# Kernel optimization log

Measured on AMD Instinct MI355X. Metric: run time of the kernel, lower is better.

Reference implementation:

```python
import jax, jax.numpy as jnp
import numpy as np

SCALE = 1.0  # alpha / rank = 32 / 32


def setup_inputs() -> dict:
    key = jax.random.key(0)
    k_x, k_w, k_b, k_a, k_bb = jax.random.split(key, 5)
    B, S, D = 4, 4096, 3072
    depth, rank = 4, 32
    x = jax.random.normal(k_x, (B, S, D), dtype=jnp.float32)
    W = jax.random.normal(k_w, (D, D), dtype=jnp.float32) * (1.0 / np.sqrt(D))
    b = jax.random.normal(k_b, (D,), dtype=jnp.float32) * 0.02
    lora_A = jax.random.normal(k_a, (depth, rank, D), dtype=jnp.float32) * (1.0 / np.sqrt(D))
    lora_B = jax.random.normal(k_bb, (depth, D, rank), dtype=jnp.float32) * 0.02
    return {"x": x, "W": W, "b": b, "lora_A": lora_A, "lora_B": lora_B}


def reference(x, W, b, lora_A, lora_B):
    # base: y = x @ W.T + b
    base_out = jnp.einsum('bsi,oi->bso', x, W) + b
    # stacked LoRA: sum_d (x @ A_d.T @ B_d.T); dropout=0 -> identity
    # down-project to rank per depth: [B,S,depth,rank]
    z = jnp.einsum('bsi,dri->bsdr', x, lora_A)
    lora_out = jnp.einsum('bsdr,dor->bso', z, lora_B)
    return base_out + lora_out * SCALE
```

## Files before the change

### kernel.cpp

```cpp
#include <hip/hip_runtime.h>
#include <hip/hip_bf16.h>


typedef unsigned short ushort_t;
typedef short bf16x8 __attribute__((ext_vector_type(8)));
typedef float floatx4 __attribute__((ext_vector_type(4)));
typedef unsigned short ushortx4 __attribute__((ext_vector_type(4)));
typedef unsigned short ushortx8 __attribute__((ext_vector_type(8)));

__device__ __forceinline__ ushort_t f2bf(float f) {
    __hip_bfloat16 h = __float2bfloat16(f);
    return *(ushort_t*)&h;
}

__device__ __forceinline__ void async_load16(const void* g, void* l) {
    __builtin_amdgcn_global_load_lds(
        (const __attribute__((address_space(1))) void*)g,
        (__attribute__((address_space(3))) void*)l,
        16, 0, 0);
}

#define MFMA16(a, b, c) __builtin_amdgcn_mfma_f32_16x16x32_bf16(a, b, c, 0, 0, 0)

__global__ __launch_bounds__(256)
void cvt_kernel(const float* __restrict__ in, ushort_t* __restrict__ out, int n8) {
    int i = blockIdx.x * 256 + threadIdx.x;
    if (i < n8) {
        const float4 v0 = ((const float4*)in)[2 * i];
        const float4 v1 = ((const float4*)in)[2 * i + 1];
        ushortx8 o = { f2bf(v0.x), f2bf(v0.y), f2bf(v0.z), f2bf(v0.w),
                       f2bf(v1.x), f2bf(v1.y), f2bf(v1.z), f2bf(v1.w) };
        ((ushortx8*)out)[i] = o;
    }
}

__global__ __launch_bounds__(256)
void transpose_lora_kernel(const float* __restrict__ lb,
                           const float* __restrict__ la,
                           ushort_t* __restrict__ outB,
                           ushort_t* __restrict__ outA) {
    int bid = blockIdx.x;
    if (bid < 1536) {
        int idx = bid * 256 + threadIdx.x;
        int n = idx >> 7;
        int j = idx & 127;
        int d = j >> 5, r = j & 31;
        outB[idx] = f2bf(lb[(size_t)d * (3072 * 32) + (size_t)n * 32 + r]);
    } else {
        int idx = (bid - 1536) * 256 + threadIdx.x;
        int kk = idx >> 7;
        int j  = idx & 127;
        outA[idx] = f2bf(la[(size_t)j * 3072 + kk]);
    }
}

template <int KT, bool OUT_F32, bool ADD_MAT>
__global__ __launch_bounds__(256)
void gemm_bt_kernel(const ushort_t* __restrict__ A, int lda,
                    const ushort_t* __restrict__ B, int ldb,
                    const float* __restrict__ Cadd,
                    const float* __restrict__ bias,
                    void* __restrict__ Cv, int ldc)
{
    __shared__ ushort_t As[128 * 32];
    __shared__ ushort_t Bs[128 * 32];

    const int t    = threadIdx.x;
    const int lane = t & 63;
    const int wave = t >> 6;
    const int wr   = wave >> 1, wc = wave & 1;
    const int quad = lane >> 4, l16 = lane & 15;

    const int mBase = blockIdx.y * 128;
    const int nBase = blockIdx.x * 128;

    floatx4 acc[4][4] = {};

    const int p0 = t,       r0 = p0 >> 2, g0 = ((p0 & 3) ^ ((r0 >> 1) & 3)) << 3;
    const int p1 = t + 256, r1 = p1 >> 2, g1 = ((p1 & 3) ^ ((r1 >> 1) & 3)) << 3;
    const int qs = (quad ^ ((l16 >> 1) & 3)) << 3;

    for (int kt = 0; kt < KT; ++kt) {
        const int ko = kt * 32;

        async_load16(A + (size_t)(mBase + r0) * lda + ko + g0, &As[p0 * 8]);
        async_load16(A + (size_t)(mBase + r1) * lda + ko + g1, &As[p1 * 8]);
        async_load16(B + (size_t)(nBase + r0) * ldb + ko + g0, &Bs[p0 * 8]);
        async_load16(B + (size_t)(nBase + r1) * ldb + ko + g1, &Bs[p1 * 8]);

        __syncthreads();

        bf16x8 af[4], bf[4];
#pragma unroll
        for (int mi = 0; mi < 4; ++mi)
            af[mi] = *(const bf16x8*)&As[(wr * 64 + mi * 16 + l16) * 32 + qs];
#pragma unroll
        for (int ni = 0; ni < 4; ++ni)
            bf[ni] = *(const bf16x8*)&Bs[(wc * 64 + ni * 16 + l16) * 32 + qs];

#pragma unroll
        for (int mi = 0; mi < 4; ++mi)
#pragma unroll
            for (int ni = 0; ni < 4; ++ni)
                acc[mi][ni] = MFMA16(af[mi], bf[ni], acc[mi][ni]);

        __syncthreads();
    }

#pragma unroll
    for (int ni = 0; ni < 4; ++ni) {
        const int col = nBase + wc * 64 + ni * 16 + l16;
        const float bv = bias ? bias[col] : 0.0f;
#pragma unroll
        for (int mi = 0; mi < 4; ++mi) {
            const int row = mBase + wr * 64 + mi * 16 + quad * 4;
#pragma unroll
            for (int r = 0; r < 4; ++r) {
                float v = acc[mi][ni][r] + bv;
                if (ADD_MAT) v += Cadd[(size_t)(row + r) * ldc + col];
                if (OUT_F32) {
                    ((float*)Cv)[(size_t)(row + r) * ldc + col] = v;
                } else {
                    ((ushort_t*)Cv)[(size_t)(row + r) * ldc + col] = f2bf(v);
                }
            }
        }
    }
}

__global__ __launch_bounds__(512)
void gemm256_kernel(const ushort_t* __restrict__ A,
                    const ushort_t* __restrict__ B,
                    const float* __restrict__ bias,
                    float* __restrict__ C)
{
    constexpr int LDA = 3072;
    constexpr int NT  = 48;
    constexpr int NBX = 12;

    __shared__ ushort_t smem_u[81920];
    char* const smem = (char*)smem_u;

    const int t    = threadIdx.x;
    const int lane = t & 63;
    const int wave = t >> 6;
    const int wr   = wave >> 2;
    const int wc   = wave & 3;
    const int quad = lane >> 4;
    const int l16  = lane & 15;

    const int bid = blockIdx.x;
    const int sw  = (bid & 7) * 96 + (bid >> 3);
    const int bx  = sw % NBX;
    const int by  = sw / NBX;
    const int mBase = by * 256;
    const int nBase = bx * 256;

    const int prow = t >> 3;
    const int cg   = (t & 7) ^ (prow & 7);
    const ushort_t* const aSrc = A + (size_t)(mBase + prow) * LDA + cg * 8;
    const ushort_t* const bSrc = B + (size_t)(nBase + prow) * LDA + cg * 8;

#define STAGE_A(off, h, ktv) do {                                           \
        const ushort_t* _s = aSrc + (size_t)(h) * 128 * LDA + (ktv) * 64;   \
        char* _d = smem + (off) + (h) * 16384 + t * 16;                     \
        async_load16(_s, _d);                                               \
        async_load16(_s + 64 * LDA, _d + 8192);                             \
    } while (0)
#define STAGE_B(off, h, ktv) do {                                           \
        const ushort_t* _s = bSrc + (size_t)(h) * 128 * LDA + (ktv) * 64;   \
        char* _d = smem + (off) + (h) * 16384 + t * 16;                     \
        async_load16(_s, _d);                                               \
        async_load16(_s + 64 * LDA, _d + 8192);                             \
    } while (0)

    const int s0  = ((0 + quad) ^ (l16 & 7)) << 4;
    const int s1  = ((4 + quad) ^ (l16 & 7)) << 4;
    const int aRdB = wr * 16384 + l16 * 128;
    const int bRdB = (wc >> 1) * 16384 + ((wc & 1) * 64 + l16) * 128;

    floatx4 acc[8][4] = {};
    bf16x8 af[8][2];
    bf16x8 bfr[4][2];

    STAGE_A(0,      0, 0); STAGE_A(0,      1, 0);
    STAGE_B(65536,  0, 0); STAGE_B(65536,  1, 0);
    STAGE_A(32768,  0, 1); STAGE_A(32768,  1, 1);
    STAGE_B(98304,  0, 1); STAGE_B(98304,  1, 1);
    asm volatile("s_waitcnt vmcnt(8)" ::: "memory");
    __builtin_amdgcn_s_barrier();
    __builtin_amdgcn_sched_barrier(0);

    int aOff = 0;
    int bRdO = 65536;
    int bStO = 131072;

    for (int kt = 0; kt < NT; ++kt) {
        const int ktN = (kt + 2 < NT) ? kt + 2 : NT - 1;

        STAGE_B(bStO, 0, ktN);
        STAGE_B(bStO, 1, ktN);
        __builtin_amdgcn_sched_barrier(0);

#pragma unroll
        for (int mi = 0; mi < 8; ++mi) {
            af[mi][0] = *(const bf16x8*)(smem + aOff + aRdB + mi * 2048 + s0);
            af[mi][1] = *(const bf16x8*)(smem + aOff + aRdB + mi * 2048 + s1);
        }
#pragma unroll
        for (int nj = 0; nj < 4; ++nj) {
            bfr[nj][0] = *(const bf16x8*)(smem + bRdO + bRdB + nj * 2048 + s0);
            bfr[nj][1] = *(const bf16x8*)(smem + bRdO + bRdB + nj * 2048 + s1);
        }
#pragma unroll
        for (int ks = 0; ks < 2; ++ks)
#pragma unroll
            for (int mi = 0; mi < 8; ++mi)
#pragma unroll
                for (int nj = 0; nj < 2; ++nj)
                    acc[mi][nj] = MFMA16(af[mi][ks], bfr[nj][ks], acc[mi][nj]);

        asm volatile("s_waitcnt lgkmcnt(0)" ::: "memory");
        __builtin_amdgcn_sched_barrier(0);
        __builtin_amdgcn_s_barrier();

        STAGE_A(aOff, 0, ktN);
        STAGE_A(aOff, 1, ktN);
        __builtin_amdgcn_sched_barrier(0);

        __builtin_amdgcn_s_setprio(1);
#pragma unroll
        for (int ks = 0; ks < 2; ++ks)
#pragma unroll
            for (int mi = 0; mi < 8; ++mi)
#pragma unroll
                for (int nj = 0; nj < 2; ++nj)
                    acc[mi][2 + nj] = MFMA16(af[mi][ks], bfr[2 + nj][ks],
                                             acc[mi][2 + nj]);
        __builtin_amdgcn_s_setprio(0);
        __builtin_amdgcn_sched_barrier(0);
        asm volatile("s_waitcnt vmcnt(8)" ::: "memory");
        __builtin_amdgcn_s_barrier();
        __builtin_amdgcn_sched_barrier(0);

        aOff ^= 32768;
        bRdO = (bRdO == 131072) ? 65536 : bRdO + 32768;
        bStO = (bStO == 131072) ? 65536 : bStO + 32768;
    }

    asm volatile("s_waitcnt vmcnt(0)" ::: "memory");

#pragma unroll
    for (int ni = 0; ni < 4; ++ni) {
        const int col = nBase + wc * 64 + ni * 16 + l16;
        const float bv = bias[col];
#pragma unroll
        for (int mi = 0; mi < 8; ++mi) {
            const int row0 = mBase + wr * 128 + mi * 16 + quad * 4;
            float* cp = C + (size_t)row0 * LDA + col;
#pragma unroll
            for (int r = 0; r < 4; ++r)
                cp[(size_t)r * LDA] = acc[mi][ni][r] + bv;
        }
    }
#undef STAGE_A
#undef STAGE_B
}

extern "C" void kernel_launch(void* const* d_in, const int* in_sizes, int n_in,
                              void* d_out, int out_size, void* d_ws, size_t ws_size,
                              hipStream_t stream) {
    const float* x  = (const float*)d_in[0];
    const float* W  = (const float*)d_in[1];
    const float* b  = (const float*)d_in[2];
    const float* lA = (const float*)d_in[3];
    const float* lB = (const float*)d_in[4];
    float* out = (float*)d_out;

    constexpr int M = 4 * 4096;
    constexpr int N = 3072;
    constexpr int K = 3072;
    constexpr size_t nX  = (size_t)M * K;
    constexpr size_t nW  = (size_t)N * K;
    constexpr size_t nT  = (size_t)128 * K;

    ushort_t* xb    = (ushort_t*)d_ws;
    ushort_t* Weffb = xb + nX;
    ushort_t* Bp    = Weffb + nW;
    ushort_t* At    = Bp + nT;

    cvt_kernel<<<nX / 8 / 256, 256, 0, stream>>>(x, xb, (int)(nX / 8));

    transpose_lora_kernel<<<2 * (nT / 256), 256, 0, stream>>>(lB, lA, Bp, At);

    gemm_bt_kernel<4, false, true><<<dim3(N / 128, N / 128), 256, 0, stream>>>(
        Bp, 128, At, 128, W, nullptr, Weffb, N);

    gemm256_kernel<<<(M / 256) * (N / 256), 512, 0, stream>>>(xb, Weffb, b, out);
}
```

Baseline: 630.7 us.

## Switch main GEMM inner loop from 16x16x32 to 32x32x16 bf16 MFMA

Replaces the 16x16x32 MFMA tiling with 32x32x16 MFMA instructions. Each wave now computes a 128x64 tile as 4x2 32x32 blocks, and the LDS fragment addressing and swizzle offsets are recomputed to match the 32-lane layout. The larger MFMA shape needs fewer LDS fragment reads per FLOP and fewer instructions. The cost is a changed register and LDS read pattern, a different split of B loads between the two phases, and an epilogue that stores rows in strided groups.

Result: slower. 648.2 us (+2.8%).

```diff
diff --git a/kernel.cpp b/kernel.cpp
--- a/kernel.cpp
+++ b/kernel.cpp
@@ -5,6 +5,7 @@
 typedef unsigned short ushort_t;
 typedef short bf16x8 __attribute__((ext_vector_type(8)));
 typedef float floatx4 __attribute__((ext_vector_type(4)));
+typedef float floatx16 __attribute__((ext_vector_type(16)));
 typedef unsigned short ushortx4 __attribute__((ext_vector_type(4)));
 typedef unsigned short ushortx8 __attribute__((ext_vector_type(8)));
 
@@ -21,6 +22,7 @@
 }
 
 #define MFMA16(a, b, c) __builtin_amdgcn_mfma_f32_16x16x32_bf16(a, b, c, 0, 0, 0)
+#define MFMA32(a, b, c) __builtin_amdgcn_mfma_f32_32x32x16_bf16(a, b, c, 0, 0, 0)
 
 __global__ __launch_bounds__(256)
 void cvt_kernel(const float* __restrict__ in, ushort_t* __restrict__ out, int n8) {
@@ -146,8 +148,8 @@
     const int wave = t >> 6;
     const int wr   = wave >> 2;
     const int wc   = wave & 3;
-    const int quad = lane >> 4;
-    const int l16  = lane & 15;
+    const int l32  = lane & 31;
+    const int hi   = lane >> 5;
 
     const int bid = blockIdx.x;
     const int sw  = (bid & 7) * 96 + (bid >> 3);
@@ -174,14 +176,19 @@
         async_load16(_s + 64 * LDA, _d + 8192);                             \
     } while (0)
 
-    const int s0  = ((0 + quad) ^ (l16 & 7)) << 4;
-    const int s1  = ((4 + quad) ^ (l16 & 7)) << 4;
-    const int aRdB = wr * 16384 + l16 * 128;
-    const int bRdB = (wc >> 1) * 16384 + ((wc & 1) * 64 + l16) * 128;
-
-    floatx4 acc[8][4] = {};
-    bf16x8 af[8][2];
-    bf16x8 bfr[4][2];
+    const int q = hi ^ (l32 & 7);
+    const int sx0 = ((0 ^ q)) << 4;
+    const int sx1 = ((2 ^ q)) << 4;
+    const int sx2 = ((4 ^ q)) << 4;
+    const int sx3 = ((6 ^ q)) << 4;
+    const int sxk[4] = { sx0, sx1, sx2, sx3 };
+
+    const int aRdB = wr * 16384 + l32 * 128;
+    const int bRdB = (wc >> 1) * 16384 + ((wc & 1) * 64 + l32) * 128;
+
+    floatx16 acc[4][2] = {};
+    bf16x8 af[4][4];
+    bf16x8 bf0[4], bf1[4];
 
     STAGE_A(0,      0, 0); STAGE_A(0,      1, 0);
     STAGE_B(65536,  0, 0); STAGE_B(65536,  1, 0);
@@ -203,22 +210,19 @@
         __builtin_amdgcn_sched_barrier(0);
 
 #pragma unroll
-        for (int mi = 0; mi < 8; ++mi) {
-            af[mi][0] = *(const bf16x8*)(smem + aOff + aRdB + mi * 2048 + s0);
-            af[mi][1] = *(const bf16x8*)(smem + aOff + aRdB + mi * 2048 + s1);
-        }
-#pragma unroll
-        for (int nj = 0; nj < 4; ++nj) {
-            bfr[nj][0] = *(const bf16x8*)(smem + bRdO + bRdB + nj * 2048 + s0);
-            bfr[nj][1] = *(const bf16x8*)(smem + bRdO + bRdB + nj * 2048 + s1);
-        }
-#pragma unroll
-        for (int ks = 0; ks < 2; ++ks)
-#pragma unroll
-            for (int mi = 0; mi < 8; ++mi)
-#pragma unroll
-                for (int nj = 0; nj < 2; ++nj)
-                    acc[mi][nj] = MFMA16(af[mi][ks], bfr[nj][ks], acc[mi][nj]);
+        for (int ks = 0; ks < 4; ++ks)
+            bf0[ks] = *(const bf16x8*)(smem + bRdO + bRdB + sxk[ks]);
+#pragma unroll
+        for (int mi = 0; mi < 4; ++mi)
+#pragma unroll
+            for (int ks = 0; ks < 4; ++ks)
+                af[mi][ks] = *(const bf16x8*)(smem + aOff + aRdB + mi * 4096 + sxk[ks]);
+
+#pragma unroll
+        for (int ks = 0; ks < 4; ++ks)
+#pragma unroll
+            for (int mi = 0; mi < 4; ++mi)
+                acc[mi][0] = MFMA32(af[mi][ks], bf0[ks], acc[mi][0]);
 
         asm volatile("s_waitcnt lgkmcnt(0)" ::: "memory");
         __builtin_amdgcn_sched_barrier(0);
@@ -230,13 +234,13 @@
 
         __builtin_amdgcn_s_setprio(1);
 #pragma unroll
-        for (int ks = 0; ks < 2; ++ks)
-#pragma unroll
-            for (int mi = 0; mi < 8; ++mi)
-#pragma unroll
-                for (int nj = 0; nj < 2; ++nj)
-                    acc[mi][2 + nj] = MFMA16(af[mi][ks], bfr[2 + nj][ks],
-                                             acc[mi][2 + nj]);
+        for (int ks = 0; ks < 4; ++ks)
+            bf1[ks] = *(const bf16x8*)(smem + bRdO + bRdB + 4096 + sxk[ks]);
+#pragma unroll
+        for (int ks = 0; ks < 4; ++ks)
+#pragma unroll
+            for (int mi = 0; mi < 4; ++mi)
+                acc[mi][1] = MFMA32(af[mi][ks], bf1[ks], acc[mi][1]);
         __builtin_amdgcn_s_setprio(0);
         __builtin_amdgcn_sched_barrier(0);
         asm volatile("s_waitcnt vmcnt(8)" ::: "memory");
@@ -251,16 +255,17 @@
     asm volatile("s_waitcnt vmcnt(0)" ::: "memory");
 
 #pragma unroll
-    for (int ni = 0; ni < 4; ++ni) {
-        const int col = nBase + wc * 64 + ni * 16 + l16;
+    for (int nj = 0; nj < 2; ++nj) {
+        const int col = nBase + wc * 64 + nj * 32 + l32;
         const float bv = bias[col];
 #pragma unroll
-        for (int mi = 0; mi < 8; ++mi) {
-            const int row0 = mBase + wr * 128 + mi * 16 + quad * 4;
-            float* cp = C + (size_t)row0 * LDA + col;
-#pragma unroll
-            for (int r = 0; r < 4; ++r)
-                cp[(size_t)r * LDA] = acc[mi][ni][r] + bv;
+        for (int mi = 0; mi < 4; ++mi) {
+            const int row0 = mBase + wr * 128 + mi * 32 + 4 * hi;
+#pragma unroll
+            for (int reg = 0; reg < 16; ++reg) {
+                const int row = row0 + (reg & 3) + 8 * (reg >> 2);
+                C[(size_t)row * LDA + col] = acc[mi][nj][reg] + bv;
+            }
         }
     }
 #undef STAGE_A
```
